# Performance work log

Hardware: AMD Instinct MI355X
Metric: run time of the kernel (lower is better)

The kernel has to match this reference:

```python
import jax, jax.numpy as jnp
import numpy as np
from jax import lax

HIDDEN = 64
N_POS = 32  # intra-frame positions, fixed by split_video

def _split_video(v):
    # view(4,4,10,8,8) -> permute(1,3,0,2,4) -> [4,8,4,10,8] -> reshape [32,4,10,8]
    return v.reshape(4, 4, 10, 8, 8).transpose(1, 3, 0, 2, 4).reshape(N_POS, 4, 10, 8)

def _encode(x, w, b):
    # Conv2d(4, hidden, 3, padding=1) + ReLU + AdaptiveAvgPool2d(1)
    y = lax.conv_general_dilated(x, w, (1, 1), 'SAME',
                                 dimension_numbers=('NCHW', 'OIHW', 'NCHW'))
    y = jax.nn.relu(y + b[None, :, None, None])
    return y.mean(axis=(2, 3))  # [N, hidden]

def _greedy_assign(pref, k):
    # Stable greedy: rounds r=0..31, patches pid=0..k-1 in order; first free
    def body(i, state):
        assign, taken = state
        pid = i % k
        pos = pref[pid, i // k]
        do = (assign[pid] < 0) & (~taken[pos])
        assign = assign.at[pid].set(jnp.where(do, pos, assign[pid]))
        taken = taken.at[pos].set(taken[pos] | do)
        return assign, taken
    init = (jnp.full((k,), -1, jnp.int32), jnp.zeros((N_POS,), bool))
    assign, _ = lax.fori_loop(0, N_POS * k, body, init)
    return assign

def setup_inputs() -> dict:
    key = jax.random.key(0)
    ks = jax.random.split(key, 5)
    k = 32
    return {
        'v_latent': jax.random.normal(ks[0], (4, 4, 10, 8, 8), jnp.float32),
        'p_tensor': jax.random.normal(ks[1], (k, 4, 10, 8), jnp.float32),
        'p_old_idx': jax.random.randint(ks[2], (k,), 0, N_POS),
        'v_w': jax.random.normal(ks[3], (HIDDEN, 4, 3, 3), jnp.float32) * 0.1,
        'v_b': jnp.zeros((HIDDEN,), jnp.float32),
        'p_w': jax.random.normal(ks[4], (HIDDEN, 4, 3, 3), jnp.float32) * 0.1,
        'p_b': jnp.zeros((HIDDEN,), jnp.float32),
    }

def reference(v_latent, p_tensor, p_old_idx, v_w, v_b, p_w, p_b):
    k = p_tensor.shape[0]
    v_emb = _encode(_split_video(v_latent), v_w, v_b)  # [32, hidden]
    p_emb = _encode(p_tensor, p_w, p_b)                # [k, hidden]
    scores = p_emb @ v_emb.T                           # [k, 32]
    pref = jnp.argsort(-scores, axis=-1)               # descending sort indices
    return _greedy_assign(pref, k)                     # [k] int32 positions
```

## Files before the change

kernel.cpp:

```cpp
#include <hip/hip_runtime.h>
#include <hip/hip_bf16.h>


#define HIDDEN 64
#define NPOS 32

__global__ __launch_bounds__(256) void encode_kernel(
    const float* __restrict__ v_latent,
    const float* __restrict__ p_tensor,
    const float* __restrict__ v_w,
    const float* __restrict__ v_b,
    const float* __restrict__ p_w,
    const float* __restrict__ p_b,
    float* __restrict__ emb)
{
    __shared__ float xpad[4][12][10];
    __shared__ float partial[4][64];

    const int n   = blockIdx.x;
    const int tid = threadIdx.x;
    const bool is_video = (n < 32);

    const float* w    = is_video ? v_w : p_w;
    const float* bias = is_video ? v_b : p_b;

    for (int s = tid; s < 480; s += 256) {
        const int ic  = s / 120;
        const int rem = s % 120;
        const int r   = rem / 10;
        const int col = rem % 10;
        float val = 0.f;
        if (r >= 1 && r <= 10 && col >= 1 && col <= 8) {
            const int h = r - 1, ww = col - 1;
            if (is_video) {
                const int b = n >> 3, d = n & 7;
                val = v_latent[ic * 2560 + b * 640 + h * 64 + d * 8 + ww];
            } else {
                val = p_tensor[(n - 32) * 320 + ic * 80 + h * 8 + ww];
            }
        }
        xpad[ic][r][col] = val;
    }

    const int oc  = tid & 63;
    const int seg = tid >> 6;

    float wr[36];
#pragma unroll
    for (int i = 0; i < 36; i++) wr[i] = w[oc * 36 + i];
    const float bval = bias[oc];

    __syncthreads();

    float sum = 0.f;
#pragma unroll
    for (int pp = 0; pp < 20; pp++) {
        const int p = seg * 20 + pp;
        const int h = p >> 3;
        const int wcol = p & 7;
        float acc = bval;
#pragma unroll
        for (int ic = 0; ic < 4; ic++)
#pragma unroll
            for (int kh = 0; kh < 3; kh++)
#pragma unroll
                for (int kw = 0; kw < 3; kw++)
                    acc += xpad[ic][h + kh][wcol + kw] * wr[ic * 9 + kh * 3 + kw];
        sum += fmaxf(acc, 0.f);
    }
    partial[seg][oc] = sum;
    __syncthreads();

    if (seg == 0) {
        const float t = partial[0][oc] + partial[1][oc] + partial[2][oc] + partial[3][oc];
        emb[n * 64 + oc] = t * (1.f / 80.f);
    }
}

__global__ __launch_bounds__(64) void match_kernel(
    const float* __restrict__ emb,
    int* __restrict__ out)
{
    __shared__ float ve[32][65];
    __shared__ float pe[32][65];
    __shared__ float sc[32][33];
    __shared__ int   pref[32][32];
    __shared__ int   claim[32];
    __shared__ int   taken[32];

    const int tid = threadIdx.x;

    for (int i = tid; i < 2048; i += 64) {
        const int r = i >> 6, c = i & 63;
        ve[r][c] = emb[i];
        pe[r][c] = emb[2048 + i];
    }
    __syncthreads();

    for (int t = tid; t < 1024; t += 64) {
        const int p = t >> 5, v = t & 31;
        float acc = 0.f;
#pragma unroll
        for (int h = 0; h < 64; h++)
            acc += pe[p][h] * ve[v][h];
        sc[p][v] = acc;
    }
    __syncthreads();

    for (int t = tid; t < 1024; t += 64) {
        const int p = t >> 5, v = t & 31;
        const float s = sc[p][v];
        int r = 0;
#pragma unroll
        for (int u = 0; u < 32; u++) {
            const float su = sc[p][u];
            r += (su > s) || (su == s && u < v);
        }
        pref[p][r] = v;
    }
    if (tid < 32) { claim[tid] = 64; taken[tid] = 0; }
    __syncthreads();

    int assign = -1;
    for (int r = 0; r < 32; r++) {
        int pos = 0;
        bool want = false;
        if (tid < 32 && assign < 0) {
            pos = pref[tid][r];
            if (!taken[pos]) {
                want = true;
                atomicMin(&claim[pos], tid);
            }
        }
        __syncthreads();
        if (want && claim[pos] == tid) {
            assign = pos;
            taken[pos] = 1;
            claim[pos] = 64;
        }
        __syncthreads();
    }

    if (tid < 32) out[tid] = assign;
}

extern "C" void kernel_launch(void* const* d_in, const int* in_sizes, int n_in,
                              void* d_out, int out_size, void* d_ws, size_t ws_size,
                              hipStream_t stream) {
    const float* v_latent = (const float*)d_in[0];
    const float* p_tensor = (const float*)d_in[1];
    const float* v_w = (const float*)d_in[3];
    const float* v_b = (const float*)d_in[4];
    const float* p_w = (const float*)d_in[5];
    const float* p_b = (const float*)d_in[6];

    int*   out = (int*)d_out;
    float* emb = (float*)d_ws;

    encode_kernel<<<64, 256, 0, stream>>>(v_latent, p_tensor, v_w, v_b, p_w, p_b, emb);
    match_kernel<<<1, 64, 0, stream>>>(emb, out);
}
```

Baseline: 101.5 us.

## Fuse encode and match kernels via last-block atomic counter

Merges the encoder and matching kernels into one launch. The last block to finish, found with an atomic counter and threadfence, runs the scoring, sort and greedy assignment using 256 threads instead of 64. Weight loads are also vectorised to float4. This drops one kernel launch but adds a memset launch and raises per-block shared memory, which may lower occupancy.

```diff
diff --git a/kernel.cpp b/kernel.cpp
--- a/kernel.cpp
+++ b/kernel.cpp
@@ -5,17 +5,26 @@
 #define HIDDEN 64
 #define NPOS 32
 
-__global__ __launch_bounds__(256) void encode_kernel(
+__global__ __launch_bounds__(256) void fused_kernel(
     const float* __restrict__ v_latent,
     const float* __restrict__ p_tensor,
     const float* __restrict__ v_w,
     const float* __restrict__ v_b,
     const float* __restrict__ p_w,
     const float* __restrict__ p_b,
-    float* __restrict__ emb)
+    float* emb,
+    int*   counter,
+    int* __restrict__ out)
 {
     __shared__ float xpad[4][12][10];
     __shared__ float partial[4][64];
+    __shared__ int   last_flag;
+    __shared__ float ve[32][65];
+    __shared__ float pe[32][65];
+    __shared__ float sc[32][33];
+    __shared__ int   pref[32][32];
+    __shared__ int   claim[32];
+    __shared__ int   taken[32];
 
     const int n   = blockIdx.x;
     const int tid = threadIdx.x;
@@ -46,8 +55,15 @@
     const int seg = tid >> 6;
 
     float wr[36];
+    {
+        const float4* w4 = (const float4*)(w + oc * 36);
 #pragma unroll
-    for (int i = 0; i < 36; i++) wr[i] = w[oc * 36 + i];
+        for (int i = 0; i < 9; i++) {
+            const float4 q = w4[i];
+            wr[i * 4 + 0] = q.x; wr[i * 4 + 1] = q.y;
+            wr[i * 4 + 2] = q.z; wr[i * 4 + 3] = q.w;
+        }
+    }
     const float bval = bias[oc];
 
     __syncthreads();
@@ -56,8 +72,7 @@
 #pragma unroll
     for (int pp = 0; pp < 20; pp++) {
         const int p = seg * 20 + pp;
-        const int h = p >> 3;
-        const int wcol = p & 7;
+        const int h = p >> 3, wcol = p & 7;
         float acc = bval;
 #pragma unroll
         for (int ic = 0; ic < 4; ic++)
@@ -75,29 +90,26 @@
         const float t = partial[0][oc] + partial[1][oc] + partial[2][oc] + partial[3][oc];
         emb[n * 64 + oc] = t * (1.f / 80.f);
     }
-}
+    __syncthreads();
 
-__global__ __launch_bounds__(64) void match_kernel(
-    const float* __restrict__ emb,
-    int* __restrict__ out)
-{
-    __shared__ float ve[32][65];
-    __shared__ float pe[32][65];
-    __shared__ float sc[32][33];
-    __shared__ int   pref[32][32];
-    __shared__ int   claim[32];
-    __shared__ int   taken[32];
+    if (tid == 0) {
+        __threadfence();
+        const int old = atomicAdd(counter, 1);
+        last_flag = (old == 63);
+        if (last_flag) __threadfence();
+    }
+    __syncthreads();
+    if (!last_flag) return;
 
-    const int tid = threadIdx.x;
-
-    for (int i = tid; i < 2048; i += 64) {
+    for (int i = tid; i < 2048; i += 256) {
         const int r = i >> 6, c = i & 63;
         ve[r][c] = emb[i];
         pe[r][c] = emb[2048 + i];
     }
+    if (tid < 32) { claim[tid] = 64; taken[tid] = 0; }
     __syncthreads();
 
-    for (int t = tid; t < 1024; t += 64) {
+    for (int t = tid; t < 1024; t += 256) {
         const int p = t >> 5, v = t & 31;
         float acc = 0.f;
 #pragma unroll
@@ -107,7 +119,7 @@
     }
     __syncthreads();
 
-    for (int t = tid; t < 1024; t += 64) {
+    for (int t = tid; t < 1024; t += 256) {
         const int p = t >> 5, v = t & 31;
         const float s = sc[p][v];
         int r = 0;
@@ -118,7 +130,6 @@
         }
         pref[p][r] = v;
     }
-    if (tid < 32) { claim[tid] = 64; taken[tid] = 0; }
     __syncthreads();
 
     int assign = -1;
@@ -154,9 +165,11 @@
     const float* p_w = (const float*)d_in[5];
     const float* p_b = (const float*)d_in[6];
 
-    int*   out = (int*)d_out;
-    float* emb = (float*)d_ws;
+    int*   out     = (int*)d_out;
+    float* emb     = (float*)d_ws;
+    int*   counter = (int*)((char*)d_ws + 64 * 64 * 4);
 
-    encode_kernel<<<64, 256, 0, stream>>>(v_latent, p_tensor, v_w, v_b, p_w, p_b, emb);
-    match_kernel<<<1, 64, 0, stream>>>(emb, out);
+    hipMemsetAsync(counter, 0, sizeof(int), stream);
+    fused_kernel<<<64, 256, 0, stream>>>(v_latent, p_tensor, v_w, v_b, p_w, p_b,
+                                         emb, counter, out);
 }
```

Measured after the change: 82.85 us. 18.4% less time.
